# Performance work log

Hardware: AMD Instinct MI355X
Metric: run time of the kernel (lower is better)

The kernel has to match this reference:

```python
import jax, jax.numpy as jnp
import numpy as np

B, S, D, H = 2, 2048, 1024, 16
DK = D // H

def setup_inputs() -> dict:
    key = jax.random.key(0)
    ks = jax.random.split(key, 8)
    scale = 1.0 / np.sqrt(D)
    return {
        "Q_in": jax.random.normal(ks[0], (B, S, D), jnp.float32),
        "K_in": jax.random.normal(ks[1], (B, S, D), jnp.float32),
        "V_in": jax.random.normal(ks[2], (B, S, D), jnp.float32),
        "Wq": jax.random.normal(ks[3], (D, D), jnp.float32) * scale,
        "bq": jnp.zeros((D,), jnp.float32),
        "Wk": jax.random.normal(ks[4], (D, D), jnp.float32) * scale,
        "bk": jnp.zeros((D,), jnp.float32),
        "Wv": jax.random.normal(ks[5], (D, D), jnp.float32) * scale,
        "bv": jnp.zeros((D,), jnp.float32),
        "Wo": jax.random.normal(ks[6], (D, D), jnp.float32) * scale,
        "bo": jnp.zeros((D,), jnp.float32),
    }

def _split_heads(x):
    # [B, S, D] -> [B, H, S, DK]
    b, s, _ = x.shape
    return x.reshape(b, s, H, DK).transpose(0, 2, 1, 3)

def reference(Q_in, K_in, V_in, Wq, bq, Wk, bk, Wv, bv, Wo, bo):
    q = _split_heads(Q_in @ Wq + bq)  # [B,H,S,DK]
    k = _split_heads(K_in @ Wk + bk)
    v = _split_heads(V_in @ Wv + bv)
    scores = jnp.einsum('bhqd,bhkd->bhqk', q, k) / jnp.sqrt(jnp.float32(DK))
    attn = jax.nn.softmax(scores, axis=-1)  # [B,H,S,S]
    out = jnp.einsum('bhqk,bhkd->bhqd', attn, v)  # [B,H,S,DK]
    out = out.transpose(0, 2, 1, 3).reshape(Q_in.shape[0], -1, D)  # [B,S,D]
    out = out @ Wo + bo
    return out, attn
```

## Files before the change

kernel.cpp:

```cpp
#include <hip/hip_runtime.h>
#include <hip/hip_bf16.h>
#include <cstdint>
#include <cstddef>

#define B_  2
#define S_  2048
#define D_  1024
#define H_  16
#define DK_ 64

typedef _Float16 half8 __attribute__((ext_vector_type(8)));
typedef _Float16 half4v __attribute__((ext_vector_type(4)));
typedef float floatx4 __attribute__((ext_vector_type(4)));

#define AS1 __attribute__((address_space(1)))
#define AS3 __attribute__((address_space(3)))

__device__ __forceinline__ half8 ld_half8(const _Float16* p) {
    return *reinterpret_cast<const half8*>(p);
}

#define MFMA16(a, b, c) __builtin_amdgcn_mfma_f32_16x16x32_f16((a), (b), (c), 0, 0, 0)

__global__ void k_f32_to_f16(const float* __restrict__ src, _Float16* __restrict__ dst, int n4) {
    int i = blockIdx.x * blockDim.x + threadIdx.x;
    if (i >= n4) return;
    float4 v = reinterpret_cast<const float4*>(src)[i];
    half4v o;
    o[0] = (_Float16)v.x; o[1] = (_Float16)v.y; o[2] = (_Float16)v.z; o[3] = (_Float16)v.w;
    *reinterpret_cast<half4v*>(dst + 4 * (size_t)i) = o;
}

__global__ void k_wtrans(const float* __restrict__ W0, const float* __restrict__ W1,
                         const float* __restrict__ W2, const float* __restrict__ W3,
                         _Float16* __restrict__ T0, _Float16* __restrict__ T1,
                         _Float16* __restrict__ T2, _Float16* __restrict__ T3) {
    const float* W = (blockIdx.z == 0) ? W0 : (blockIdx.z == 1) ? W1 : (blockIdx.z == 2) ? W2 : W3;
    _Float16*    T = (blockIdx.z == 0) ? T0 : (blockIdx.z == 1) ? T1 : (blockIdx.z == 2) ? T2 : T3;
    __shared__ float t[32][33];
    int x = blockIdx.x * 32 + threadIdx.x;
    #pragma unroll
    for (int yy = threadIdx.y; yy < 32; yy += 8) {
        t[yy][threadIdx.x] = W[(size_t)(blockIdx.y * 32 + yy) * D_ + x];
    }
    __syncthreads();
    #pragma unroll
    for (int yy = threadIdx.y; yy < 32; yy += 8) {
        T[(size_t)(blockIdx.x * 32 + yy) * D_ + blockIdx.y * 32 + threadIdx.x] =
            (_Float16)t[threadIdx.x][yy];
    }
}

__launch_bounds__(256)
__global__ void k_qkv_gemm(const _Float16* __restrict__ Xq, const _Float16* __restrict__ Xk,
                           const _Float16* __restrict__ Xv,
                           const _Float16* __restrict__ WqT, const _Float16* __restrict__ WkT,
                           const _Float16* __restrict__ WvT,
                           const float* __restrict__ bq, const float* __restrict__ bk,
                           const float* __restrict__ bv,
                           _Float16* __restrict__ qo, _Float16* __restrict__ ko,
                           _Float16* __restrict__ vTo) {
    __shared__ __align__(16) _Float16 As[128 * 32];
    __shared__ __align__(16) _Float16 Bs[128 * 32];

    const int z = blockIdx.z;
    const _Float16* X    = (z == 0) ? Xq  : (z == 1) ? Xk  : Xv;
    const _Float16* WT   = (z == 0) ? WqT : (z == 1) ? WkT : WvT;
    const float*    bias = (z == 0) ? bq  : (z == 1) ? bk  : bv;

    const int tid = threadIdx.x;
    const int lane = tid & 63, wave = tid >> 6;
    const int lr = lane & 15, q4 = lane >> 4;
    const int wr = wave >> 1, wc = wave & 1;
    const int m0 = blockIdx.y * 128;
    const int n0 = blockIdx.x * 128;

    const int c0 = tid, c1 = tid + 256;
    const _Float16* aS0 = X  + (size_t)(m0 + (c0 >> 2)) * D_ + (c0 & 3) * 8;
    const _Float16* aS1 = X  + (size_t)(m0 + (c1 >> 2)) * D_ + (c1 & 3) * 8;
    const _Float16* bS0 = WT + (size_t)(n0 + (c0 >> 2)) * D_ + (c0 & 3) * 8;
    const _Float16* bS1 = WT + (size_t)(n0 + (c1 >> 2)) * D_ + (c1 & 3) * 8;
    _Float16* aD0 = As + c0 * 8;  _Float16* aD1 = As + c1 * 8;
    _Float16* bD0 = Bs + c0 * 8;  _Float16* bD1 = Bs + c1 * 8;

    floatx4 acc[4][4];
    #pragma unroll
    for (int mt = 0; mt < 4; mt++)
        #pragma unroll
        for (int nt = 0; nt < 4; nt++)
            acc[mt][nt] = (floatx4){0.f, 0.f, 0.f, 0.f};

    for (int k0 = 0; k0 < D_; k0 += 32) {
        __builtin_amdgcn_global_load_lds((const AS1 void*)(aS0 + k0), (AS3 void*)aD0, 16, 0, 0);
        __builtin_amdgcn_global_load_lds((const AS1 void*)(aS1 + k0), (AS3 void*)aD1, 16, 0, 0);
        __builtin_amdgcn_global_load_lds((const AS1 void*)(bS0 + k0), (AS3 void*)bD0, 16, 0, 0);
        __builtin_amdgcn_global_load_lds((const AS1 void*)(bS1 + k0), (AS3 void*)bD1, 16, 0, 0);
        __syncthreads();
        half8 af[4], bf[4];
        #pragma unroll
        for (int mt = 0; mt < 4; mt++)
            af[mt] = *reinterpret_cast<const half8*>(As + (size_t)(wr * 64 + mt * 16 + lr) * 32 + q4 * 8);
        #pragma unroll
        for (int nt = 0; nt < 4; nt++)
            bf[nt] = *reinterpret_cast<const half8*>(Bs + (size_t)(wc * 64 + nt * 16 + lr) * 32 + q4 * 8);
        #pragma unroll
        for (int mt = 0; mt < 4; mt++)
            #pragma unroll
            for (int nt = 0; nt < 4; nt++)
                acc[mt][nt] = MFMA16(af[mt], bf[nt], acc[mt][nt]);
        __syncthreads();
    }

    #pragma unroll
    for (int mt = 0; mt < 4; mt++) {
        #pragma unroll
        for (int nt = 0; nt < 4; nt++) {
            int gn = n0 + wc * 64 + nt * 16 + lr;
            float bval = bias[gn];
            int h = gn >> 6, dk = gn & 63;
            #pragma unroll
            for (int r = 0; r < 4; r++) {
                int gm = m0 + wr * 64 + mt * 16 + q4 * 4 + r;
                float val = acc[mt][nt][r] + bval;
                int b = gm >> 11, s = gm & (S_ - 1);
                if (z == 0) {
                    qo[(((size_t)b * H_ + h) * S_ + s) * DK_ + dk] = (_Float16)(val * 0.125f);
                } else if (z == 1) {
                    ko[(((size_t)b * H_ + h) * S_ + s) * DK_ + dk] = (_Float16)val;
                } else {
                    vTo[(((size_t)b * H_ + h) * DK_ + dk) * S_ + s] = (_Float16)val;
                }
            }
        }
    }
}

__launch_bounds__(256)
__global__ void k_attn(const _Float16* __restrict__ q, const _Float16* __restrict__ k,
                       const _Float16* __restrict__ vT,
                       float* __restrict__ attn, _Float16* __restrict__ oh) {
    __shared__ __align__(16) _Float16 plds[4][16][40];
    __shared__ float sums[2][2][16];
    __shared__ __align__(16) float ocomb[2][64][16];

    const int bh = blockIdx.y;
    const int lane = threadIdx.x & 63, wave = threadIdx.x >> 6;
    const int qt = wave >> 1, jh = wave & 1;
    const int lr = lane & 15, q4 = lane >> 4;
    const int i0 = blockIdx.x * 32 + qt * 16;
    const int jbase = jh * (S_ / 2);

    const _Float16* qb = q + (size_t)bh * S_ * DK_;
    const _Float16* kb = k + (size_t)bh * S_ * DK_;
    const _Float16* vb = vT + (size_t)bh * DK_ * S_;

    half8 qf0 = ld_half8(qb + (size_t)(i0 + lr) * DK_ + q4 * 8);
    half8 qf1 = ld_half8(qb + (size_t)(i0 + lr) * DK_ + 32 + q4 * 8);

    float psum = 0.f;
    for (int jc = jbase; jc < jbase + S_ / 2; jc += 16) {
        const _Float16* krow = kb + (size_t)(jc + lr) * DK_ + q4 * 8;
        half8 kf0 = ld_half8(krow);
        half8 kf1 = ld_half8(krow + 32);
        floatx4 s = {0.f, 0.f, 0.f, 0.f};
        s = MFMA16(kf0, qf0, s);
        s = MFMA16(kf1, qf1, s);
        psum += __expf(s[0]) + __expf(s[1]) + __expf(s[2]) + __expf(s[3]);
    }
    psum += __shfl_xor(psum, 16);
    psum += __shfl_xor(psum, 32);
    if (q4 == 0) sums[qt][jh][lr] = psum;
    __syncthreads();
    const float inv = 1.0f / (sums[qt][0][lr] + sums[qt][1][lr]);

    floatx4 oacc[4];
    #pragma unroll
    for (int nt = 0; nt < 4; nt++) oacc[nt] = (floatx4){0.f, 0.f, 0.f, 0.f};
    float* arow = attn + (size_t)bh * S_ * S_ + (size_t)(i0 + lr) * S_;

    for (int j0 = jbase; j0 < jbase + S_ / 2; j0 += 32) {
        #pragma unroll
        for (int c = 0; c < 2; c++) {
            const int jc = j0 + c * 16;
            const _Float16* krow = kb + (size_t)(jc + lr) * DK_ + q4 * 8;
            half8 kf0 = ld_half8(krow);
            half8 kf1 = ld_half8(krow + 32);
            floatx4 s = {0.f, 0.f, 0.f, 0.f};
            s = MFMA16(kf0, qf0, s);
            s = MFMA16(kf1, qf1, s);
            floatx4 p;
            p[0] = __expf(s[0]) * inv;
            p[1] = __expf(s[1]) * inv;
            p[2] = __expf(s[2]) * inv;
            p[3] = __expf(s[3]) * inv;
            __builtin_nontemporal_store(p, reinterpret_cast<floatx4*>(arow + jc + q4 * 4));
            half4v ph;
            ph[0] = (_Float16)p[0]; ph[1] = (_Float16)p[1];
            ph[2] = (_Float16)p[2]; ph[3] = (_Float16)p[3];
            *reinterpret_cast<half4v*>(&plds[wave][lr][c * 16 + q4 * 4]) = ph;
        }
        __threadfence_block();
        half8 pa = *reinterpret_cast<const half8*>(&plds[wave][lr][q4 * 8]);
        #pragma unroll
        for (int nt = 0; nt < 4; nt++) {
            half8 vv = ld_half8(vb + (size_t)(nt * 16 + lr) * S_ + j0 + q4 * 8);
            oacc[nt] = MFMA16(pa, vv, oacc[nt]);
        }
    }

    if (jh == 1) {
        #pragma unroll
        for (int nt = 0; nt < 4; nt++)
            *reinterpret_cast<floatx4*>(&ocomb[qt][lane][nt * 4]) = oacc[nt];
    }
    __syncthreads();
    if (jh == 0) {
        const int b = bh >> 4, h = bh & 15;
        #pragma unroll
        for (int nt = 0; nt < 4; nt++) {
            oacc[nt] += *reinterpret_cast<const floatx4*>(&ocomb[qt][lane][nt * 4]);
            #pragma unroll
            for (int r = 0; r < 4; r++) {
                oh[((size_t)b * S_ + i0 + q4 * 4 + r) * D_ + h * DK_ + nt * 16 + lr] =
                    (_Float16)oacc[nt][r];
            }
        }
    }
}

__launch_bounds__(256)
__global__ void k_out_gemm(const _Float16* __restrict__ X, const _Float16* __restrict__ WT,
                           const float* __restrict__ bias, float* __restrict__ out) {
    __shared__ __align__(16) _Float16 As[128 * 32];
    __shared__ __align__(16) _Float16 Bs[128 * 32];

    const int tid = threadIdx.x;
    const int lane = tid & 63, wave = tid >> 6;
    const int lr = lane & 15, q4 = lane >> 4;
    const int wr = wave >> 1, wc = wave & 1;
    const int m0 = blockIdx.y * 128;
    const int n0 = blockIdx.x * 128;

    const int c0 = tid, c1 = tid + 256;
    const _Float16* aS0 = X  + (size_t)(m0 + (c0 >> 2)) * D_ + (c0 & 3) * 8;
    const _Float16* aS1 = X  + (size_t)(m0 + (c1 >> 2)) * D_ + (c1 & 3) * 8;
    const _Float16* bS0 = WT + (size_t)(n0 + (c0 >> 2)) * D_ + (c0 & 3) * 8;
    const _Float16* bS1 = WT + (size_t)(n0 + (c1 >> 2)) * D_ + (c1 & 3) * 8;
    _Float16* aD0 = As + c0 * 8;  _Float16* aD1 = As + c1 * 8;
    _Float16* bD0 = Bs + c0 * 8;  _Float16* bD1 = Bs + c1 * 8;

    floatx4 acc[4][4];
    #pragma unroll
    for (int mt = 0; mt < 4; mt++)
        #pragma unroll
        for (int nt = 0; nt < 4; nt++)
            acc[mt][nt] = (floatx4){0.f, 0.f, 0.f, 0.f};

    for (int k0 = 0; k0 < D_; k0 += 32) {
        __builtin_amdgcn_global_load_lds((const AS1 void*)(aS0 + k0), (AS3 void*)aD0, 16, 0, 0);
        __builtin_amdgcn_global_load_lds((const AS1 void*)(aS1 + k0), (AS3 void*)aD1, 16, 0, 0);
        __builtin_amdgcn_global_load_lds((const AS1 void*)(bS0 + k0), (AS3 void*)bD0, 16, 0, 0);
        __builtin_amdgcn_global_load_lds((const AS1 void*)(bS1 + k0), (AS3 void*)bD1, 16, 0, 0);
        __syncthreads();
        half8 af[4], bf[4];
        #pragma unroll
        for (int mt = 0; mt < 4; mt++)
            af[mt] = *reinterpret_cast<const half8*>(As + (size_t)(wr * 64 + mt * 16 + lr) * 32 + q4 * 8);
        #pragma unroll
        for (int nt = 0; nt < 4; nt++)
            bf[nt] = *reinterpret_cast<const half8*>(Bs + (size_t)(wc * 64 + nt * 16 + lr) * 32 + q4 * 8);
        #pragma unroll
        for (int mt = 0; mt < 4; mt++)
            #pragma unroll
            for (int nt = 0; nt < 4; nt++)
                acc[mt][nt] = MFMA16(af[mt], bf[nt], acc[mt][nt]);
        __syncthreads();
    }

    #pragma unroll
    for (int mt = 0; mt < 4; mt++) {
        #pragma unroll
        for (int nt = 0; nt < 4; nt++) {
            int gn = n0 + wc * 64 + nt * 16 + lr;
            float bval = bias[gn];
            #pragma unroll
            for (int r = 0; r < 4; r++) {
                int gm = m0 + wr * 64 + mt * 16 + q4 * 4 + r;
                out[(size_t)gm * D_ + gn] = acc[mt][nt][r] + bval;
            }
        }
    }
}

extern "C" void kernel_launch(void* const* d_in, const int* in_sizes, int n_in,
                              void* d_out, int out_size, void* d_ws, size_t ws_size,
                              hipStream_t stream) {
    const float* Q_in = (const float*)d_in[0];
    const float* K_in = (const float*)d_in[1];
    const float* V_in = (const float*)d_in[2];
    const float* Wq = (const float*)d_in[3];
    const float* bq = (const float*)d_in[4];
    const float* Wk = (const float*)d_in[5];
    const float* bk = (const float*)d_in[6];
    const float* Wv = (const float*)d_in[7];
    const float* bv = (const float*)d_in[8];
    const float* Wo = (const float*)d_in[9];
    const float* bo = (const float*)d_in[10];

    const size_t NEL = (size_t)B_ * S_ * D_;
    _Float16* Xhq = (_Float16*)d_ws;
    _Float16* Xhk = Xhq + NEL;
    _Float16* Xhv = Xhk + NEL;
    _Float16* WqT = Xhv + NEL;
    _Float16* WkT = WqT + (size_t)D_ * D_;
    _Float16* WvT = WkT + (size_t)D_ * D_;
    _Float16* WoT = WvT + (size_t)D_ * D_;
    _Float16* qh  = WoT + (size_t)D_ * D_;
    _Float16* kh  = qh + NEL;
    _Float16* vTh = kh + NEL;
    _Float16* ohh = vTh + NEL;

    float* out  = (float*)d_out;
    float* attn = out + NEL;

    const int n4 = (int)(NEL / 4);
    dim3 cvtg((n4 + 255) / 256);
    k_f32_to_f16<<<cvtg, 256, 0, stream>>>(Q_in, Xhq, n4);
    k_f32_to_f16<<<cvtg, 256, 0, stream>>>(K_in, Xhk, n4);
    k_f32_to_f16<<<cvtg, 256, 0, stream>>>(V_in, Xhv, n4);

    k_wtrans<<<dim3(32, 32, 4), dim3(32, 8), 0, stream>>>(Wq, Wk, Wv, Wo, WqT, WkT, WvT, WoT);

    k_qkv_gemm<<<dim3(D_ / 128, (B_ * S_) / 128, 3), 256, 0, stream>>>(
        Xhq, Xhk, Xhv, WqT, WkT, WvT, bq, bk, bv, qh, kh, vTh);

    k_attn<<<dim3(S_ / 32, B_ * H_), 256, 0, stream>>>(qh, kh, vTh, attn, ohh);

    k_out_gemm<<<dim3(D_ / 128, (B_ * S_) / 128), 256, 0, stream>>>(ohh, WoT, bo, out);
}
```

Baseline: 936.8 us.

## Cache unnormalized exp scores in LDS to avoid recomputing QK^T in attention

```diff
diff --git a/kernel.cpp b/kernel.cpp
--- a/kernel.cpp
+++ b/kernel.cpp
@@ -139,16 +139,19 @@
 __global__ void k_attn(const _Float16* __restrict__ q, const _Float16* __restrict__ k,
                        const _Float16* __restrict__ vT,
                        float* __restrict__ attn, _Float16* __restrict__ oh) {
-    __shared__ __align__(16) _Float16 plds[4][16][40];
-    __shared__ float sums[2][2][16];
-    __shared__ __align__(16) float ocomb[2][64][16];
-
-    const int bh = blockIdx.y;
-    const int lane = threadIdx.x & 63, wave = threadIdx.x >> 6;
-    const int qt = wave >> 1, jh = wave & 1;
+    extern __shared__ _Float16 smem[];
+    _Float16* P   = smem;
+    float* psums  = (float*)(smem + 16 * 2048);
+    float* invs   = psums + 64;
+
+    const int rawid = blockIdx.y * gridDim.x + blockIdx.x;
+    const int v = (rawid & 7) * 512 + (rawid >> 3);
+    const int bh = v >> 7;
+    const int i0 = (v & 127) * 16;
+
+    const int lane = threadIdx.x & 63, w = threadIdx.x >> 6;
     const int lr = lane & 15, q4 = lane >> 4;
-    const int i0 = blockIdx.x * 32 + qt * 16;
-    const int jbase = jh * (S_ / 2);
+    const int swz = (lr & 7) << 3;
 
     const _Float16* qb = q + (size_t)bh * S_ * DK_;
     const _Float16* kb = k + (size_t)bh * S_ * DK_;
@@ -158,73 +161,61 @@
     half8 qf1 = ld_half8(qb + (size_t)(i0 + lr) * DK_ + 32 + q4 * 8);
 
     float psum = 0.f;
-    for (int jc = jbase; jc < jbase + S_ / 2; jc += 16) {
+    const int jc0 = w * 512;
+    #pragma unroll 2
+    for (int jc = jc0; jc < jc0 + 512; jc += 16) {
         const _Float16* krow = kb + (size_t)(jc + lr) * DK_ + q4 * 8;
         half8 kf0 = ld_half8(krow);
         half8 kf1 = ld_half8(krow + 32);
         floatx4 s = {0.f, 0.f, 0.f, 0.f};
         s = MFMA16(kf0, qf0, s);
         s = MFMA16(kf1, qf1, s);
-        psum += __expf(s[0]) + __expf(s[1]) + __expf(s[2]) + __expf(s[3]);
+        float e0 = __expf(s[0]), e1 = __expf(s[1]), e2 = __expf(s[2]), e3 = __expf(s[3]);
+        psum += (e0 + e1) + (e2 + e3);
+        half4v ph;
+        ph[0] = (_Float16)e0; ph[1] = (_Float16)e1;
+        ph[2] = (_Float16)e2; ph[3] = (_Float16)e3;
+        *reinterpret_cast<half4v*>(&P[(lr * 2048 + jc + q4 * 4) ^ swz]) = ph;
     }
     psum += __shfl_xor(psum, 16);
     psum += __shfl_xor(psum, 32);
-    if (q4 == 0) sums[qt][jh][lr] = psum;
+    if (q4 == 0) psums[w * 16 + lr] = psum;
     __syncthreads();
-    const float inv = 1.0f / (sums[qt][0][lr] + sums[qt][1][lr]);
-
-    floatx4 oacc[4];
-    #pragma unroll
-    for (int nt = 0; nt < 4; nt++) oacc[nt] = (floatx4){0.f, 0.f, 0.f, 0.f};
-    float* arow = attn + (size_t)bh * S_ * S_ + (size_t)(i0 + lr) * S_;
-
-    for (int j0 = jbase; j0 < jbase + S_ / 2; j0 += 32) {
-        #pragma unroll
-        for (int c = 0; c < 2; c++) {
-            const int jc = j0 + c * 16;
-            const _Float16* krow = kb + (size_t)(jc + lr) * DK_ + q4 * 8;
-            half8 kf0 = ld_half8(krow);
-            half8 kf1 = ld_half8(krow + 32);
-            floatx4 s = {0.f, 0.f, 0.f, 0.f};
-            s = MFMA16(kf0, qf0, s);
-            s = MFMA16(kf1, qf1, s);
-            floatx4 p;
-            p[0] = __expf(s[0]) * inv;
-            p[1] = __expf(s[1]) * inv;
-            p[2] = __expf(s[2]) * inv;
-            p[3] = __expf(s[3]) * inv;
-            __builtin_nontemporal_store(p, reinterpret_cast<floatx4*>(arow + jc + q4 * 4));
-            half4v ph;
-            ph[0] = (_Float16)p[0]; ph[1] = (_Float16)p[1];
-            ph[2] = (_Float16)p[2]; ph[3] = (_Float16)p[3];
-            *reinterpret_cast<half4v*>(&plds[wave][lr][c * 16 + q4 * 4]) = ph;
+
+    if (threadIdx.x < 16)
+        invs[threadIdx.x] = 1.0f / (psums[threadIdx.x] + psums[16 + threadIdx.x] +
+                                    psums[32 + threadIdx.x] + psums[48 + threadIdx.x]);
+    __syncthreads();
+
+    {
+        const int r = w * 4 + q4;
+        const float myinv = invs[r];
+        const int rsw = (r & 7) << 3;
+        float* arow = attn + (size_t)bh * S_ * S_ + (size_t)(i0 + r) * S_;
+        #pragma unroll 4
+        for (int i = 0; i < 32; i++) {
+            int col = i * 64 + lr * 4;
+            half4v ph = *reinterpret_cast<const half4v*>(&P[(r * 2048 + col) ^ rsw]);
+            floatx4 pv;
+            pv[0] = (float)ph[0] * myinv; pv[1] = (float)ph[1] * myinv;
+            pv[2] = (float)ph[2] * myinv; pv[3] = (float)ph[3] * myinv;
+            __builtin_nontemporal_store(pv, reinterpret_cast<floatx4*>(arow + col));
         }
-        __threadfence_block();
-        half8 pa = *reinterpret_cast<const half8*>(&plds[wave][lr][q4 * 8]);
-        #pragma unroll
-        for (int nt = 0; nt < 4; nt++) {
-            half8 vv = ld_half8(vb + (size_t)(nt * 16 + lr) * S_ + j0 + q4 * 8);
-            oacc[nt] = MFMA16(pa, vv, oacc[nt]);
-        }
-    }
-
-    if (jh == 1) {
-        #pragma unroll
-        for (int nt = 0; nt < 4; nt++)
-            *reinterpret_cast<floatx4*>(&ocomb[qt][lane][nt * 4]) = oacc[nt];
-    }
-    __syncthreads();
-    if (jh == 0) {
-        const int b = bh >> 4, h = bh & 15;
-        #pragma unroll
-        for (int nt = 0; nt < 4; nt++) {
-            oacc[nt] += *reinterpret_cast<const floatx4*>(&ocomb[qt][lane][nt * 4]);
-            #pragma unroll
-            for (int r = 0; r < 4; r++) {
-                oh[((size_t)b * S_ + i0 + q4 * 4 + r) * D_ + h * DK_ + nt * 16 + lr] =
-                    (_Float16)oacc[nt][r];
-            }
-        }
+    }
+
+    floatx4 oacc = {0.f, 0.f, 0.f, 0.f};
+    const _Float16* vrow = vb + (size_t)(w * 16 + lr) * S_ + q4 * 8;
+    #pragma unroll 4
+    for (int j0 = 0; j0 < S_; j0 += 32) {
+        half8 pa = *reinterpret_cast<const half8*>(&P[(lr * 2048 + j0 + q4 * 8) ^ swz]);
+        half8 vv = ld_half8(vrow + j0);
+        oacc = MFMA16(pa, vv, oacc);
+    }
+    const int b = bh >> 4, h = bh & 15;
+    #pragma unroll
+    for (int r = 0; r < 4; r++) {
+        float val = oacc[r] * invs[q4 * 4 + r];
+        oh[((size_t)b * S_ + i0 + q4 * 4 + r) * D_ + h * DK_ + w * 16 + lr] = (_Float16)val;
     }
 }
 
@@ -334,7 +325,8 @@
     k_qkv_gemm<<<dim3(D_ / 128, (B_ * S_) / 128, 3), 256, 0, stream>>>(
         Xhq, Xhk, Xhv, WqT, WkT, WvT, bq, bk, bv, qh, kh, vTh);
 
-    k_attn<<<dim3(S_ / 32, B_ * H_), 256, 0, stream>>>(qh, kh, vTh, attn, ohh);
+    const size_t attn_lds = 16 * 2048 * sizeof(_Float16) + 80 * sizeof(float);
+    k_attn<<<dim3(S_ / 16, B_ * H_), 256, attn_lds, stream>>>(qh, kh, vTh, attn, ohh);
 
     k_out_gemm<<<dim3(D_ / 128, (B_ * S_) / 128), 256, 0, stream>>>(ohh, WoT, bo, out);
 }
```

After: 836.0 us. -10.8%, faster.
